# Kernel optimization log

Hardware: AMD Instinct MI355X
Metric: run time of the kernel (lower is better)

Reference implementation:

```python
import jax, jax.numpy as jnp
import numpy as np

B, F, N, J, L_LAYERS = 16, 16, 1024, 8, 3


def setup_inputs() -> dict:
    key = jax.random.key(0)
    k1, k2, k3 = jax.random.split(key, 3)
    x = jax.random.normal(k1, (B, F, N), dtype=jnp.float32)
    psi = jax.random.normal(k2, (J, N, N), dtype=jnp.float32) / np.sqrt(N)
    lowpass = jax.random.uniform(k3, (N,), dtype=jnp.float32) / N
    return {"x": x, "psi": psi, "lowpass": lowpass, "L": L_LAYERS}


def reference(x, psi, lowpass, L):
    # x: [B, F, N] graph signals; psi: [J, N, N] wavelet filterbank; lowpass: [N]
    Bs, Fs, Ns = x.shape
    # layer-0 lowpass projection: phi = x @ lowpass -> [B, F, 1]
    phi = jnp.einsum('bfn,n->bf', x, lowpass)[:, :, None]
    S_x = x[:, None, :, :]  # [B, K=1, F, N]
    for _ in range(1, L):
        # apply all J wavelets to all K branches, then abs nonlinearity
        # (branch order k-major, j-minor matches the torch cat loop)
        S_x = jnp.abs(jnp.einsum('bkfn,jnm->bkjfm', S_x, psi))
        K = S_x.shape[1] * S_x.shape[2]
        S_x = S_x.reshape(Bs, K, Fs, Ns)
        # lowpass-pool every branch: [B, F, K]
        phi_l = jnp.einsum('bkfn,n->bfk', S_x, lowpass)
        phi = jnp.concatenate([phi, phi_l], axis=2)
    return phi  # [B, F, 1 + J + J^2 + ... + J^(L-1)]
```

## Files before the change

### kernel.cpp

```cpp
#include <hip/hip_runtime.h>

#define ND 1024
#define NNE (ND*ND)

typedef float f32x4 __attribute__((ext_vector_type(4)));
typedef int i32x4 __attribute__((ext_vector_type(4)));
typedef int i32x8 __attribute__((ext_vector_type(8)));

__device__ __forceinline__ void gload_lds16(const void* g, void* l) {
  __builtin_amdgcn_global_load_lds(
      (const __attribute__((address_space(1))) void*)g,
      (__attribute__((address_space(3))) void*)l, 16, 0, 0);
}

__global__ __launch_bounds__(256)
void prep_kernel(const float* __restrict__ psi, unsigned char* __restrict__ out8,
                 const float* __restrict__ x, const float* __restrict__ lp,
                 unsigned char* __restrict__ x8, float* __restrict__ phi) {
  __shared__ __align__(16) unsigned char T[128 * 144];
  __shared__ float ws[4];
  const int blk = blockIdx.x;
  const int tid = threadIdx.x;

  if (blk >= 512) {
    int row = blk - 512;
    if (tid >= 1 && tid < 73) phi[row * 73 + tid] = 0.f;
    float4 v = reinterpret_cast<const float4*>(x + (size_t)row * ND)[tid];
    float4 l = reinterpret_cast<const float4*>(lp)[tid];
    int pk = __builtin_amdgcn_cvt_pk_fp8_f32(v.x, v.y, 0, false);
    pk = __builtin_amdgcn_cvt_pk_fp8_f32(v.z, v.w, pk, true);
    reinterpret_cast<unsigned int*>(x8 + (size_t)row * ND)[tid] = (unsigned int)pk;
    float s = v.x * l.x + v.y * l.y + v.z * l.z + v.w * l.w;
    #pragma unroll
    for (int off = 32; off; off >>= 1) s += __shfl_xor(s, off);
    if ((tid & 63) == 0) ws[tid >> 6] = s;
    __syncthreads();
    if (tid == 0) phi[row * 73] = ws[0] + ws[1] + ws[2] + ws[3];
    return;
  }

  const int j  = blk >> 6;
  const int t6 = blk & 63;
  const int tn = t6 >> 3, tm = t6 & 7;
  const int n0 = tn * 128, m0 = tm * 128;
  const float* src = psi + ((size_t)j << 20) + (size_t)n0 * ND + m0;

  const int rgrp = tid >> 5;
  const int c4   = (tid & 31) << 2;
  #pragma unroll
  for (int it = 0; it < 16; ++it) {
    int nl = it * 8 + rgrp;
    float4 v = *reinterpret_cast<const float4*>(src + (size_t)nl * ND + c4);
    int p01 = __builtin_amdgcn_cvt_pk_fp8_f32(v.x, v.y, 0, false);
    int p23 = __builtin_amdgcn_cvt_pk_fp8_f32(v.z, v.w, 0, false);
    T[(c4 + 0) * 144 + nl] = (unsigned char)(p01 & 0xff);
    T[(c4 + 1) * 144 + nl] = (unsigned char)((p01 >> 8) & 0xff);
    T[(c4 + 2) * 144 + nl] = (unsigned char)(p23 & 0xff);
    T[(c4 + 3) * 144 + nl] = (unsigned char)((p23 >> 8) & 0xff);
  }
  __syncthreads();

  unsigned char* dst = out8 + ((size_t)j << 20) + (size_t)m0 * ND + n0;
  const int mrow = tid >> 3;
  const int ch   = (tid & 7) << 4;
  #pragma unroll
  for (int it = 0; it < 4; ++it) {
    int ml = it * 32 + mrow;
    uint4 v = *reinterpret_cast<const uint4*>(&T[ml * 144 + ch]);
    *reinterpret_cast<uint4*>(dst + (size_t)ml * ND + ch) = v;
  }
}

__device__ __forceinline__ i32x8 dsr_frag8(const unsigned char* base, int r, int l4) {
  int s0 = l4 * 2;
  i32x4 lo = *reinterpret_cast<const i32x4*>(base + r * 128 + ((s0 ^ (r & 7)) << 4));
  i32x4 hi = *reinterpret_cast<const i32x4*>(base + r * 128 + (((s0 + 1) ^ (r & 7)) << 4));
  return __builtin_shufflevector(lo, hi, 0, 1, 2, 3, 4, 5, 6, 7);
}

__device__ __forceinline__ void stage128(const unsigned char* __restrict__ A, int row0,
                                         const unsigned char* __restrict__ Bj, int n0,
                                         int k0, unsigned char* As, unsigned char* Bs,
                                         int tid) {
  #pragma unroll
  for (int p = 0; p < 4; ++p) {
    int c = p * 256 + tid;
    int r = c >> 3;
    int s = (c & 7) ^ (r & 7);
    gload_lds16(A + (size_t)(row0 + r) * ND + k0 + (s << 4), As + c * 16);
  }
  #pragma unroll
  for (int p = 0; p < 4; ++p) {
    int c = p * 256 + tid;
    int r = c >> 3;
    int s = (c & 7) ^ (r & 7);
    gload_lds16(Bj + (size_t)(n0 + r) * ND + k0 + (s << 4), Bs + c * 16);
  }
}

__device__ __forceinline__ void compute128(const unsigned char* As, const unsigned char* Bs,
                                           f32x4 (&acc)[4][4],
                                           int wrow, int wcol, int l15, int l4) {
  i32x8 a[4], b[4];
  #pragma unroll
  for (int m = 0; m < 4; ++m)
    a[m] = dsr_frag8(As, wrow * 64 + m * 16 + l15, l4);
  #pragma unroll
  for (int n = 0; n < 4; ++n)
    b[n] = dsr_frag8(Bs, wcol * 64 + n * 16 + l15, l4);
  #pragma unroll
  for (int m = 0; m < 4; ++m)
    #pragma unroll
    for (int n = 0; n < 4; ++n)
      acc[m][n] = __builtin_amdgcn_mfma_scale_f32_16x16x128_f8f6f4(
          a[m], b[n], acc[m][n], 0, 0, 0, 0x7f7f7f7f, 0, 0x7f7f7f7f);
}

__global__ __launch_bounds__(256, 2)
void gemm8_l1(const unsigned char* __restrict__ A,
              const unsigned char* __restrict__ BT,
              const float* __restrict__ lowpass,
              unsigned char* __restrict__ Sout,
              float* __restrict__ phi) {
  __shared__ __align__(16) unsigned char As0[128 * 128];
  __shared__ __align__(16) unsigned char As1[128 * 128];
  __shared__ __align__(16) unsigned char Bs0[128 * 128];
  __shared__ __align__(16) unsigned char Bs1[128 * 128];

  const int tid  = threadIdx.x;
  const int lane = tid & 63;
  const int w    = tid >> 6;
  const int wrow = w >> 1, wcol = w & 1;
  const int l15  = lane & 15, l4 = lane >> 4;

  const int wg = blockIdx.x;
  const int j  = wg & 7;
  const int t  = wg >> 3;
  const int mtile = t & 1, ntile = t >> 1;
  const int row0 = mtile * 128, n0 = ntile * 128;
  const unsigned char* Bj = BT + (size_t)j * NNE;

  f32x4 acc[4][4] = {};

  stage128(A, row0, Bj, n0, 0, As0, Bs0, tid);
  __syncthreads();

  #pragma unroll 1
  for (int k0 = 0; k0 < ND; k0 += 128) {
    const int cur = (k0 >> 7) & 1;
    const unsigned char* Ac = cur ? As1 : As0;
    const unsigned char* Bc = cur ? Bs1 : Bs0;
    if (k0 + 128 < ND)
      stage128(A, row0, Bj, n0, k0 + 128, cur ? As0 : As1, cur ? Bs0 : Bs1, tid);
    compute128(Ac, Bc, acc, wrow, wcol, l15, l4);
    __syncthreads();
  }

  float lp[4];
  #pragma unroll
  for (int n = 0; n < 4; ++n)
    lp[n] = lowpass[n0 + wcol * 64 + n * 16 + l15];

  #pragma unroll
  for (int m = 0; m < 4; ++m) {
    #pragma unroll
    for (int r = 0; r < 4; ++r) {
      int rg = row0 + wrow * 64 + m * 16 + l4 * 4 + r;
      float psum = 0.f;
      #pragma unroll
      for (int n = 0; n < 4; ++n) {
        float v = fabsf(acc[m][n][r]);
        psum += v * lp[n];
        int colg = n0 + wcol * 64 + n * 16 + l15;
        size_t si = ((size_t)((rg >> 4) * 8 + j) * 16 + (rg & 15)) * ND + colg;
        int pk = __builtin_amdgcn_cvt_pk_fp8_f32(v, v, 0, false);
        Sout[si] = (unsigned char)(pk & 0xff);
      }
      psum += __shfl_xor(psum, 1);
      psum += __shfl_xor(psum, 2);
      psum += __shfl_xor(psum, 4);
      psum += __shfl_xor(psum, 8);
      if (l15 == 0) {
        int pidx = rg * 73 + 1 + j;
        atomicAdd(&phi[pidx], psum);
      }
    }
  }
}

__global__ __launch_bounds__(256, 2)
void gemm8_l2(const unsigned char* __restrict__ A,
              const unsigned char* __restrict__ BT,
              const float* __restrict__ lowpass,
              float* __restrict__ phi) {
  __shared__ __align__(16) unsigned char As0[128 * 128];
  __shared__ __align__(16) unsigned char As1[128 * 128];
  __shared__ __align__(16) unsigned char Bs0[128 * 128];
  __shared__ __align__(16) unsigned char Bs1[128 * 128];

  const int tid  = threadIdx.x;
  const int lane = tid & 63;
  const int w    = tid >> 6;
  const int wrow = w >> 1, wcol = w & 1;
  const int l15  = lane & 15, l4 = lane >> 4;

  const int wg  = blockIdx.x;
  const int j   = wg & 7;
  const int idx = wg >> 3;
  const unsigned char* Bj = BT + (size_t)j * NNE;

  #pragma unroll 1
  for (int tt = 0; tt < 2; ++tt) {
    const int t = idx + tt * 64;
    const int mtile = t & 15, ntile = t >> 4;
    const int row0 = mtile * 128, n0 = ntile * 128;

    f32x4 acc[4][4] = {};

    stage128(A, row0, Bj, n0, 0, As0, Bs0, tid);
    __syncthreads();

    #pragma unroll 1
    for (int k0 = 0; k0 < ND; k0 += 128) {
      const int cur = (k0 >> 7) & 1;
      const unsigned char* Ac = cur ? As1 : As0;
      const unsigned char* Bc = cur ? Bs1 : Bs0;
      if (k0 + 128 < ND)
        stage128(A, row0, Bj, n0, k0 + 128, cur ? As0 : As1, cur ? Bs0 : Bs1, tid);
      compute128(Ac, Bc, acc, wrow, wcol, l15, l4);
      __syncthreads();
    }

    float lp[4];
    #pragma unroll
    for (int n = 0; n < 4; ++n)
      lp[n] = lowpass[n0 + wcol * 64 + n * 16 + l15];

    #pragma unroll
    for (int m = 0; m < 4; ++m) {
      #pragma unroll
      for (int r = 0; r < 4; ++r) {
        int rg = row0 + wrow * 64 + m * 16 + l4 * 4 + r;
        float psum = 0.f;
        #pragma unroll
        for (int n = 0; n < 4; ++n)
          psum += fabsf(acc[m][n][r]) * lp[n];
        psum += __shfl_xor(psum, 1);
        psum += __shfl_xor(psum, 2);
        psum += __shfl_xor(psum, 4);
        psum += __shfl_xor(psum, 8);
        if (l15 == 0) {
          int pidx = ((rg >> 7) * 16 + (rg & 15)) * 73 + 9 + ((rg >> 4) & 7) * 8 + j;
          atomicAdd(&phi[pidx], psum);
        }
      }
    }
  }
}

extern "C" void kernel_launch(void* const* d_in, const int* in_sizes, int n_in,
                              void* d_out, int out_size, void* d_ws, size_t ws_size,
                              hipStream_t stream) {
  (void)in_sizes; (void)n_in; (void)ws_size; (void)out_size;
  const float* x       = (const float*)d_in[0];
  const float* psi     = (const float*)d_in[1];
  const float* lowpass = (const float*)d_in[2];
  float* phi = (float*)d_out;

  unsigned char* x8    = (unsigned char*)d_ws;
  unsigned char* psiT8 = (unsigned char*)((char*)d_ws + (1u << 20));
  unsigned char* S1f8  = (unsigned char*)((char*)d_ws + (10u << 20));

  prep_kernel<<<768, 256, 0, stream>>>(psi, psiT8, x, lowpass, x8, phi);

  gemm8_l1<<<128, 256, 0, stream>>>(x8, psiT8, lowpass, S1f8, phi);

  gemm8_l2<<<512, 256, 0, stream>>>(S1f8, psiT8, lowpass, phi);
}
```

Baseline: 61.47 us.

## Load A fragments directly from global into registers, stage only B in LDS

The A operand of both FP8 MFMA GEMM kernels is now read straight from global memory into per-wave register fragments, double-buffered across even and odd K steps, and only B goes through LDS with async global-to-LDS loads. This halves shared memory use per block and removes the LDS reads for A. In exchange A rows are loaded redundantly by the two waves sharing a row, uncoalesced 32-byte-per-lane reads replace async LDS staging, and register pressure rises with two A fragment sets live.

```diff
diff --git a/kernel.cpp b/kernel.cpp
--- a/kernel.cpp
+++ b/kernel.cpp
@@ -78,17 +78,21 @@
   return __builtin_shufflevector(lo, hi, 0, 1, 2, 3, 4, 5, 6, 7);
 }
 
-__device__ __forceinline__ void stage128(const unsigned char* __restrict__ A, int row0,
-                                         const unsigned char* __restrict__ Bj, int n0,
-                                         int k0, unsigned char* As, unsigned char* Bs,
-                                         int tid) {
-  #pragma unroll
-  for (int p = 0; p < 4; ++p) {
-    int c = p * 256 + tid;
-    int r = c >> 3;
-    int s = (c & 7) ^ (r & 7);
-    gload_lds16(A + (size_t)(row0 + r) * ND + k0 + (s << 4), As + c * 16);
-  }
+__device__ __forceinline__ i32x8 gread_frag8(const unsigned char* g) {
+  i32x4 lo = *reinterpret_cast<const i32x4*>(g);
+  i32x4 hi = *reinterpret_cast<const i32x4*>(g + 16);
+  return __builtin_shufflevector(lo, hi, 0, 1, 2, 3, 4, 5, 6, 7);
+}
+
+__device__ __forceinline__ void loadA(i32x8 (&a)[4], const unsigned char* __restrict__ A,
+                                      int row0, int k0, int wrow, int l15, int l4) {
+  #pragma unroll
+  for (int m = 0; m < 4; ++m)
+    a[m] = gread_frag8(A + (size_t)(row0 + wrow * 64 + m * 16 + l15) * ND + k0 + l4 * 32);
+}
+
+__device__ __forceinline__ void stageB(const unsigned char* __restrict__ Bj, int n0,
+                                       int k0, unsigned char* Bs, int tid) {
   #pragma unroll
   for (int p = 0; p < 4; ++p) {
     int c = p * 256 + tid;
@@ -98,13 +102,9 @@
   }
 }
 
-__device__ __forceinline__ void compute128(const unsigned char* As, const unsigned char* Bs,
-                                           f32x4 (&acc)[4][4],
-                                           int wrow, int wcol, int l15, int l4) {
-  i32x8 a[4], b[4];
-  #pragma unroll
-  for (int m = 0; m < 4; ++m)
-    a[m] = dsr_frag8(As, wrow * 64 + m * 16 + l15, l4);
+__device__ __forceinline__ void compute128(const unsigned char* Bs, const i32x8 (&a)[4],
+                                           f32x4 (&acc)[4][4], int wcol, int l15, int l4) {
+  i32x8 b[4];
   #pragma unroll
   for (int n = 0; n < 4; ++n)
     b[n] = dsr_frag8(Bs, wcol * 64 + n * 16 + l15, l4);
@@ -122,8 +122,6 @@
               const float* __restrict__ lowpass,
               unsigned char* __restrict__ Sout,
               float* __restrict__ phi) {
-  __shared__ __align__(16) unsigned char As0[128 * 128];
-  __shared__ __align__(16) unsigned char As1[128 * 128];
   __shared__ __align__(16) unsigned char Bs0[128 * 128];
   __shared__ __align__(16) unsigned char Bs1[128 * 128];
 
@@ -141,18 +139,24 @@
   const unsigned char* Bj = BT + (size_t)j * NNE;
 
   f32x4 acc[4][4] = {};
-
-  stage128(A, row0, Bj, n0, 0, As0, Bs0, tid);
+  i32x8 aE[4], aO[4];
+
+  stageB(Bj, n0, 0, Bs0, tid);
+  loadA(aE, A, row0, 0, wrow, l15, l4);
   __syncthreads();
 
   #pragma unroll 1
-  for (int k0 = 0; k0 < ND; k0 += 128) {
-    const int cur = (k0 >> 7) & 1;
-    const unsigned char* Ac = cur ? As1 : As0;
-    const unsigned char* Bc = cur ? Bs1 : Bs0;
-    if (k0 + 128 < ND)
-      stage128(A, row0, Bj, n0, k0 + 128, cur ? As0 : As1, cur ? Bs0 : Bs1, tid);
-    compute128(Ac, Bc, acc, wrow, wcol, l15, l4);
+  for (int i = 0; i < 4; ++i) {
+    const int kB = i * 256 + 128;
+    stageB(Bj, n0, kB, Bs1, tid);
+    loadA(aO, A, row0, kB, wrow, l15, l4);
+    compute128(Bs0, aE, acc, wcol, l15, l4);
+    __syncthreads();
+    if (i < 3) {
+      stageB(Bj, n0, kB + 128, Bs0, tid);
+      loadA(aE, A, row0, kB + 128, wrow, l15, l4);
+    }
+    compute128(Bs1, aO, acc, wcol, l15, l4);
     __syncthreads();
   }
 
@@ -193,8 +197,6 @@
               const unsigned char* __restrict__ BT,
               const float* __restrict__ lowpass,
               float* __restrict__ phi) {
-  __shared__ __align__(16) unsigned char As0[128 * 128];
-  __shared__ __align__(16) unsigned char As1[128 * 128];
   __shared__ __align__(16) unsigned char Bs0[128 * 128];
   __shared__ __align__(16) unsigned char Bs1[128 * 128];
 
@@ -216,18 +218,24 @@
     const int row0 = mtile * 128, n0 = ntile * 128;
 
     f32x4 acc[4][4] = {};
-
-    stage128(A, row0, Bj, n0, 0, As0, Bs0, tid);
+    i32x8 aE[4], aO[4];
+
+    stageB(Bj, n0, 0, Bs0, tid);
+    loadA(aE, A, row0, 0, wrow, l15, l4);
     __syncthreads();
 
     #pragma unroll 1
-    for (int k0 = 0; k0 < ND; k0 += 128) {
-      const int cur = (k0 >> 7) & 1;
-      const unsigned char* Ac = cur ? As1 : As0;
-      const unsigned char* Bc = cur ? Bs1 : Bs0;
-      if (k0 + 128 < ND)
-        stage128(A, row0, Bj, n0, k0 + 128, cur ? As0 : As1, cur ? Bs0 : Bs1, tid);
-      compute128(Ac, Bc, acc, wrow, wcol, l15, l4);
+    for (int i = 0; i < 4; ++i) {
+      const int kB = i * 256 + 128;
+      stageB(Bj, n0, kB, Bs1, tid);
+      loadA(aO, A, row0, kB, wrow, l15, l4);
+      compute128(Bs0, aE, acc, wcol, l15, l4);
+      __syncthreads();
+      if (i < 3) {
+        stageB(Bj, n0, kB + 128, Bs0, tid);
+        loadA(aE, A, row0, kB + 128, wrow, l15, l4);
+      }
+      compute128(Bs1, aO, acc, wcol, l15, l4);
       __syncthreads();
     }
 
```

Measured after the change: 93.35 us. 1.52x slower.

## Enlarge layer-2 FP8 GEMM tiles to 256x256 with 512-thread blocks

Applied to the files above, without the earlier changes.

The layer-2 FP8 GEMM moves from 128x128 tiles, where each 256-thread block looped over two tiles, to one 256x256 tile per 512-thread block with 8 waves in a 2x4 layout. Each wave computes 128x64 of output, which raises data reuse per LDS fragment and halves global operand traffic per output element. In exchange, LDS use grows to 128KB per block, only 256 blocks are launched, and occupancy drops to one block per CU, which leaves less room to hide latency.

```diff
diff --git a/kernel.cpp b/kernel.cpp
--- a/kernel.cpp
+++ b/kernel.cpp
@@ -188,71 +188,104 @@
   }
 }
 
-__global__ __launch_bounds__(256, 2)
+
+__device__ __forceinline__ void stage256(const unsigned char* __restrict__ A, int row0,
+                                         const unsigned char* __restrict__ Bj, int n0,
+                                         int k0, unsigned char* As, unsigned char* Bs,
+                                         int tid) {
+  #pragma unroll
+  for (int p = 0; p < 4; ++p) {
+    int c = p * 512 + tid;
+    int r = c >> 3;
+    int s = (c & 7) ^ (r & 7);
+    gload_lds16(A + (size_t)(row0 + r) * ND + k0 + (s << 4), As + c * 16);
+  }
+  #pragma unroll
+  for (int p = 0; p < 4; ++p) {
+    int c = p * 512 + tid;
+    int r = c >> 3;
+    int s = (c & 7) ^ (r & 7);
+    gload_lds16(Bj + (size_t)(n0 + r) * ND + k0 + (s << 4), Bs + c * 16);
+  }
+}
+
+__device__ __forceinline__ void compute256(const unsigned char* As, const unsigned char* Bs,
+                                           f32x4 (&acc)[8][4],
+                                           int wrow, int wcol, int l15, int l4) {
+  i32x8 b[4];
+  #pragma unroll
+  for (int n = 0; n < 4; ++n)
+    b[n] = dsr_frag8(Bs, wcol * 64 + n * 16 + l15, l4);
+  #pragma unroll
+  for (int m = 0; m < 8; ++m) {
+    i32x8 a = dsr_frag8(As, wrow * 128 + m * 16 + l15, l4);
+    #pragma unroll
+    for (int n = 0; n < 4; ++n)
+      acc[m][n] = __builtin_amdgcn_mfma_scale_f32_16x16x128_f8f6f4(
+          a, b[n], acc[m][n], 0, 0, 0, 0x7f7f7f7f, 0, 0x7f7f7f7f);
+  }
+}
+
+__global__ __launch_bounds__(512, 1)
 void gemm8_l2(const unsigned char* __restrict__ A,
               const unsigned char* __restrict__ BT,
               const float* __restrict__ lowpass,
               float* __restrict__ phi) {
-  __shared__ __align__(16) unsigned char As0[128 * 128];
-  __shared__ __align__(16) unsigned char As1[128 * 128];
-  __shared__ __align__(16) unsigned char Bs0[128 * 128];
-  __shared__ __align__(16) unsigned char Bs1[128 * 128];
+  __shared__ __align__(16) unsigned char As0[256 * 128];
+  __shared__ __align__(16) unsigned char As1[256 * 128];
+  __shared__ __align__(16) unsigned char Bs0[256 * 128];
+  __shared__ __align__(16) unsigned char Bs1[256 * 128];
 
   const int tid  = threadIdx.x;
   const int lane = tid & 63;
   const int w    = tid >> 6;
-  const int wrow = w >> 1, wcol = w & 1;
+  const int wrow = w >> 2, wcol = w & 3;
   const int l15  = lane & 15, l4 = lane >> 4;
 
-  const int wg  = blockIdx.x;
-  const int j   = wg & 7;
-  const int idx = wg >> 3;
+  const int wg = blockIdx.x;
+  const int j  = wg & 7;
+  const int t  = wg >> 3;
+  const int mtile = t & 7, ntile = t >> 3;
+  const int row0 = mtile * 256, n0 = ntile * 256;
   const unsigned char* Bj = BT + (size_t)j * NNE;
 
+  f32x4 acc[8][4] = {};
+
+  stage256(A, row0, Bj, n0, 0, As0, Bs0, tid);
+  __syncthreads();
+
   #pragma unroll 1
-  for (int tt = 0; tt < 2; ++tt) {
-    const int t = idx + tt * 64;
-    const int mtile = t & 15, ntile = t >> 4;
-    const int row0 = mtile * 128, n0 = ntile * 128;
-
-    f32x4 acc[4][4] = {};
-
-    stage128(A, row0, Bj, n0, 0, As0, Bs0, tid);
+  for (int k0 = 0; k0 < ND; k0 += 128) {
+    const int cur = (k0 >> 7) & 1;
+    const unsigned char* Ac = cur ? As1 : As0;
+    const unsigned char* Bc = cur ? Bs1 : Bs0;
+    if (k0 + 128 < ND)
+      stage256(A, row0, Bj, n0, k0 + 128, cur ? As0 : As1, cur ? Bs0 : Bs1, tid);
+    compute256(Ac, Bc, acc, wrow, wcol, l15, l4);
     __syncthreads();
-
-    #pragma unroll 1
-    for (int k0 = 0; k0 < ND; k0 += 128) {
-      const int cur = (k0 >> 7) & 1;
-      const unsigned char* Ac = cur ? As1 : As0;
-      const unsigned char* Bc = cur ? Bs1 : Bs0;
-      if (k0 + 128 < ND)
-        stage128(A, row0, Bj, n0, k0 + 128, cur ? As0 : As1, cur ? Bs0 : Bs1, tid);
-      compute128(Ac, Bc, acc, wrow, wcol, l15, l4);
-      __syncthreads();
-    }
-
-    float lp[4];
-    #pragma unroll
-    for (int n = 0; n < 4; ++n)
-      lp[n] = lowpass[n0 + wcol * 64 + n * 16 + l15];
-
-    #pragma unroll
-    for (int m = 0; m < 4; ++m) {
+  }
+
+  float lp[4];
+  #pragma unroll
+  for (int n = 0; n < 4; ++n)
+    lp[n] = lowpass[n0 + wcol * 64 + n * 16 + l15];
+
+  #pragma unroll
+  for (int m = 0; m < 8; ++m) {
+    #pragma unroll
+    for (int r = 0; r < 4; ++r) {
+      int rg = row0 + wrow * 128 + m * 16 + l4 * 4 + r;
+      float psum = 0.f;
       #pragma unroll
-      for (int r = 0; r < 4; ++r) {
-        int rg = row0 + wrow * 64 + m * 16 + l4 * 4 + r;
-        float psum = 0.f;
-        #pragma unroll
-        for (int n = 0; n < 4; ++n)
-          psum += fabsf(acc[m][n][r]) * lp[n];
-        psum += __shfl_xor(psum, 1);
-        psum += __shfl_xor(psum, 2);
-        psum += __shfl_xor(psum, 4);
-        psum += __shfl_xor(psum, 8);
-        if (l15 == 0) {
-          int pidx = ((rg >> 7) * 16 + (rg & 15)) * 73 + 9 + ((rg >> 4) & 7) * 8 + j;
-          atomicAdd(&phi[pidx], psum);
-        }
+      for (int n = 0; n < 4; ++n)
+        psum += fabsf(acc[m][n][r]) * lp[n];
+      psum += __shfl_xor(psum, 1);
+      psum += __shfl_xor(psum, 2);
+      psum += __shfl_xor(psum, 4);
+      psum += __shfl_xor(psum, 8);
+      if (l15 == 0) {
+        int pidx = ((rg >> 7) * 16 + (rg & 15)) * 73 + 9 + ((rg >> 4) & 7) * 8 + j;
+        atomicAdd(&phi[pidx], psum);
       }
     }
   }
@@ -275,5 +308,5 @@
 
   gemm8_l1<<<128, 256, 0, stream>>>(x8, psiT8, lowpass, S1f8, phi);
 
-  gemm8_l2<<<512, 256, 0, stream>>>(S1f8, psiT8, lowpass, phi);
-}
+  gemm8_l2<<<256, 512, 0, stream>>>(S1f8, psiT8, lowpass, phi);
+}
```

Result: faster. 60.20 us, median of 2 (-2.1%).
